# Performance work log

Measured on AMD Instinct MI355X. Metric: run time of the kernel, lower is better.

## Reference

```python
import jax, jax.numpy as jnp
import numpy as np
from jax import lax

IN_DIM = 128
B, H, W = 4, 64, 64


def setup_inputs() -> dict:
    key = jax.random.key(0)
    ks = jax.random.split(key, 11)
    C = IN_DIM
    c8 = C // 8
    s = lambda k, shape, scale: jax.random.normal(k, shape, dtype=jnp.float32) * scale
    return {
        "x": s(ks[0], (B, C, H, W), 1.0),
        "x_forward": s(ks[1], (B, C, H, W), 1.0),
        "x_backward": s(ks[2], (B, C, H, W), 1.0),
        # 1x1 conv weights stored as [out, in]
        "Wq": s(ks[3], (c8, C), C ** -0.5),
        "bq": jnp.zeros((c8,), jnp.float32),
        "Wk": s(ks[4], (c8, C), C ** -0.5),
        "bk": jnp.zeros((c8,), jnp.float32),
        "Wv": s(ks[5], (C, C), C ** -0.5),
        "bv": jnp.zeros((C,), jnp.float32),
        # 3x3 conv weight [out=C, in=2C, kh, kw]
        "Wf": s(ks[6], (C, 2 * C, 3, 3), (2 * C * 9) ** -0.5),
        "bf": jnp.zeros((C,), jnp.float32),
    }


def _conv1x1(x, w, b):
    # x: [B,C,H,W], w: [O,C] -> [B,O,H,W]
    return jnp.einsum("bchw,oc->bohw", x, w) + b[None, :, None, None]


def reference(x, x_forward, x_backward, Wq, bq, Wk, bk, Wv, bv, Wf, bf):
    Bb, C, Hh, Ww = x.shape
    HW = Hh * Ww
    query = _conv1x1(x_forward, Wq, bq).reshape(Bb, -1, HW)   # [B,c8,HW]
    key = _conv1x1(x, Wk, bk).reshape(Bb, -1, HW)             # [B,c8,HW]
    value = _conv1x1(x_backward, Wv, bv).reshape(Bb, C, HW)   # [B,C,HW]

    # att_score[b, k_pos, q_pos] = key[b,:,k_pos] . query[b,:,q_pos]
    att_score = jnp.einsum("bck,bcq->bkq", key, query)        # [B,HW,HW]
    max_value = jnp.max(att_score, axis=-1)                   # [B,HW]
    idx = jnp.argmax(att_score, axis=-1)                      # [B,HW] int

    selected_value = jnp.take_along_axis(value, idx[:, None, :], axis=2)
    selected_value = selected_value.reshape(Bb, C, Hh, Ww)
    max_value = max_value.reshape(Bb, 1, Hh, Ww)

    front_res = jnp.concatenate([x, selected_value], axis=1)  # [B,2C,H,W]
    front_res = lax.conv_general_dilated(
        front_res, Wf, window_strides=(1, 1), padding="SAME",
        dimension_numbers=("NCHW", "OIHW", "NCHW"),
    ) + bf[None, :, None, None]
    front_res = front_res * max_value
    return x + front_res
```

## Files before the change

kernel.cpp:

```cpp
#include <hip/hip_runtime.h>

#define HW 4096
#define CC 128
#define MARGIN 2e-3f

typedef unsigned short ushort_t;
typedef unsigned int uint_t;
typedef __attribute__((ext_vector_type(8))) short short8;
typedef __attribute__((ext_vector_type(4))) float f32x4;

__device__ __forceinline__ float dot4(float4 a, float4 b) {
    return (a.x*b.x + a.y*b.y) + (a.z*b.z + a.w*b.w);
}

__device__ __forceinline__ ushort_t f2bf(float f) {
    union { float f; uint_t u; } cv; cv.f = f;
    uint_t r = cv.u + 0x7fffu + ((cv.u >> 16) & 1u);
    return (ushort_t)(r >> 16);
}

__device__ __forceinline__ float bf2f(ushort_t h) {
    union { uint_t u; float f; } cv; cv.u = ((uint_t)h) << 16;
    return cv.f;
}

__device__ __forceinline__ void store16(ushort_t* dst, const ushort_t* s) {
    union { ushort_t s[8]; uint4 v; } a, b;
    #pragma unroll
    for (int j = 0; j < 8; j++) { a.s[j] = s[j]; b.s[j] = s[8+j]; }
    *(uint4*)dst = a.v;
    *(uint4*)(dst + 8) = b.v;
}

__device__ __forceinline__ void gl2lds16(const ushort_t* g, ushort_t* l) {
    __builtin_amdgcn_global_load_lds(
        (const __attribute__((address_space(1))) unsigned int*)g,
        (__attribute__((address_space(3))) unsigned int*)l, 16, 0, 0);
}

__global__ __launch_bounds__(256) void prep_kernel(
    const float* __restrict__ x, const float* __restrict__ xf, const float* __restrict__ xb,
    const float* __restrict__ Wq, const float* __restrict__ bq,
    const float* __restrict__ Wk, const float* __restrict__ bk,
    const float* __restrict__ Wv, const float* __restrict__ bv,
    const float* __restrict__ Wf,
    float* __restrict__ Qt, float* __restrict__ Kt, float* __restrict__ V,
    ushort_t* __restrict__ Qs, ushort_t* __restrict__ KB,
    ushort_t* __restrict__ xsel, ushort_t* __restrict__ Wt)
{
    __shared__ __align__(16) unsigned char smem[16704];
    int bid = blockIdx.x;
    int tid = threadIdx.x;

    if (bid < 32) {
        float* sW = (float*)smem;
        float* sB = sW + 2048;
        bool isQ = bid < 16;
        const float* src  = isQ ? xf : x;
        const float* W    = isQ ? Wq : Wk;
        const float* bias = isQ ? bq : bk;
        int sub = bid & 15;
        int b = sub >> 2, pt = sub & 3;
        for (int e = tid; e < 2048; e += 256) sW[e] = W[e];
        if (tid < 16) sB[tid] = bias[tid];
        __syncthreads();

        int p = pt*1024 + tid*4;
        const float* sp = src + (size_t)b * CC * HW + p;

        float4 acc[16];
        #pragma unroll
        for (int o = 0; o < 16; o++) { float bb = sB[o]; acc[o] = make_float4(bb,bb,bb,bb); }

        for (int c4 = 0; c4 < 128; c4 += 4) {
            float4 x0 = *(const float4*)&sp[(c4+0)*HW];
            float4 x1 = *(const float4*)&sp[(c4+1)*HW];
            float4 x2 = *(const float4*)&sp[(c4+2)*HW];
            float4 x3 = *(const float4*)&sp[(c4+3)*HW];
            #pragma unroll
            for (int o = 0; o < 16; o++) {
                float4 w = *(const float4*)&sW[o*128 + c4];
                acc[o].x += w.x*x0.x + w.y*x1.x + w.z*x2.x + w.w*x3.x;
                acc[o].y += w.x*x0.y + w.y*x1.y + w.z*x2.y + w.w*x3.y;
                acc[o].z += w.x*x0.z + w.y*x1.z + w.z*x2.z + w.w*x3.z;
                acc[o].w += w.x*x0.w + w.y*x1.w + w.z*x2.w + w.w*x3.w;
            }
        }

        float* dstF = isQ ? Qt : Kt;
        int pg = b*4096 + p;
        #pragma unroll
        for (int pp = 0; pp < 4; pp++) {
            float vd[16];
            #pragma unroll
            for (int o = 0; o < 16; o++)
                vd[o] = (pp==0) ? acc[o].x : (pp==1) ? acc[o].y : (pp==2) ? acc[o].z : acc[o].w;
            float4* df = (float4*)(dstF + (size_t)(pg + pp)*16);
            df[0] = make_float4(vd[0],vd[1],vd[2],vd[3]);
            df[1] = make_float4(vd[4],vd[5],vd[6],vd[7]);
            df[2] = make_float4(vd[8],vd[9],vd[10],vd[11]);
            df[3] = make_float4(vd[12],vd[13],vd[14],vd[15]);
            ushort_t h[16], m[16], l[16];
            #pragma unroll
            for (int d = 0; d < 16; d++) {
                h[d] = f2bf(vd[d]);
                float r1 = vd[d] - bf2f(h[d]);
                m[d] = f2bf(r1);
                l[d] = f2bf(r1 - bf2f(m[d]));
            }
            if (isQ) {
                ushort_t* o_ = Qs + (size_t)(pg + pp)*64;
                store16(o_,      h);
                store16(o_ + 16, m);
                store16(o_ + 32, h);
                store16(o_ + 48, l);
            } else {
                int k = p + pp;
                int u = b*256 + (k >> 4);
                int n = k & 15;
                ushort_t* o_ = KB + (size_t)u*1536 + n*32;
                store16(o_,        h); store16(o_ + 16,   h);
                store16(o_ + 512,  m); store16(o_ + 528,  m);
                store16(o_ + 1024, l); store16(o_ + 1040, h);
            }
        }
    } else if (bid < 160) {
        float* sW = (float*)smem;
        int vbid = bid - 32;
        int b = vbid >> 5, og = (vbid >> 3) & 3, pt = vbid & 7;
        for (int e = tid; e < 4096; e += 256) sW[e] = Wv[og*4096 + e];
        __syncthreads();

        int oz = tid >> 7, pz = tid & 127;
        int p = pt*512 + pz*4;
        const float* sp = xb + (size_t)b * CC * HW + p;

        float4 acc[16];
        #pragma unroll
        for (int j = 0; j < 16; j++) acc[j] = make_float4(0.f,0.f,0.f,0.f);

        for (int c4 = 0; c4 < 128; c4 += 4) {
            float4 x0 = *(const float4*)&sp[(c4+0)*HW];
            float4 x1 = *(const float4*)&sp[(c4+1)*HW];
            float4 x2 = *(const float4*)&sp[(c4+2)*HW];
            float4 x3 = *(const float4*)&sp[(c4+3)*HW];
            #pragma unroll
            for (int j = 0; j < 16; j++) {
                float4 w = *(const float4*)&sW[(oz*16 + j)*128 + c4];
                acc[j].x += w.x*x0.x + w.y*x1.x + w.z*x2.x + w.w*x3.x;
                acc[j].y += w.x*x0.y + w.y*x1.y + w.z*x2.y + w.w*x3.y;
                acc[j].z += w.x*x0.z + w.y*x1.z + w.z*x2.z + w.w*x3.z;
                acc[j].w += w.x*x0.w + w.y*x1.w + w.z*x2.w + w.w*x3.w;
            }
        }
        #pragma unroll
        for (int j = 0; j < 16; j++) {
            int o = og*32 + oz*16 + j;
            float bb = bv[o];
            float4 r = make_float4(acc[j].x+bb, acc[j].y+bb, acc[j].z+bb, acc[j].w+bb);
            *(float4*)&V[(((size_t)b*CC + o)<<12) + p] = r;
        }
    } else if (bid < 416) {
        ushort_t* sT = (ushort_t*)smem;
        int xbid = bid - 160;
        int b = xbid >> 6, y = xbid & 63;
        int cq = tid >> 6, xx = tid & 63;
        const float* src = x + ((size_t)b << 19) + (y << 6) + xx;
        #pragma unroll 4
        for (int k = 0; k < 32; k++) {
            int c = cq*32 + k;
            sT[xx*130 + c] = f2bf(src[(size_t)c << 12]);
        }
        __syncthreads();
        uint_t* dst = (uint_t*)(xsel + ((size_t)(b*4356 + (y+1)*66 + 1))*256);
        #pragma unroll
        for (int k = 0; k < 16; k++) {
            int idx = k*256 + tid;
            int s = idx >> 6, u = idx & 63;
            uint_t v = *(const uint_t*)&sT[s*130 + u*2];
            dst[s*128 + u] = v;
        }
    } else if (bid < 546) {
        int g = (bid - 416) * 256 + tid;
        if (g < 33280) {
            int b = g / 8320;
            int rem = g - b * 8320;
            int si = rem >> 5;
            int ch = rem & 31;
            int y, xx;
            if (si < 66)      { y = 0;  xx = si; }
            else if (si < 132){ y = 65; xx = si - 66; }
            else { int t = si - 132; y = 1 + (t >> 1); xx = (t & 1) ? 65 : 0; }
            int site = y * 66 + xx;
            uint4* dst = (uint4*)(xsel + ((size_t)(b*4356 + site))*256);
            dst[ch] = make_uint4(0,0,0,0);
        }
    } else {
        int t = (bid - 546) * 256 + tid;
        if (t < 36864) {
            int cg = t & 3;
            int o = (t >> 2) & 31;
            int tc = t >> 7;
            int tap = tc % 9;
            int rest = tc / 9;
            int cb = rest & 7, og = rest >> 3;
            union { ushort_t s[8]; uint4 v; } pk;
            #pragma unroll
            for (int j = 0; j < 8; j++) {
                int ci = cg*8 + j;
                pk.s[j] = f2bf(Wf[(size_t)(og*32 + o)*2304 + (cb*32 + ci)*9 + tap]);
            }
            *(uint4*)(Wt + (size_t)t*8) = pk.v;
        }
    }
}

__global__ __launch_bounds__(512) void att_kernel(
    const ushort_t* __restrict__ Qs, const ushort_t* __restrict__ KB,
    float* __restrict__ pm1, int* __restrict__ pi1, float* __restrict__ pm2)
{
    __shared__ float sM1[64*33];
    __shared__ int   sI1[64*33];
    __shared__ float sM2[64*33];

    int bid = blockIdx.x;
    int qh = bid & 1, kg = (bid >> 1) & 63, b = bid >> 7;
    int tid = threadIdx.x;
    int wave = tid >> 6, lane = tid & 63;
    int l15 = lane & 15, quad = lane >> 4;

    short8 Bf[4][3];
    const ushort_t* kb = KB + ((size_t)((b*256 + kg*4)*3))*512 + l15*32 + quad*8;
    #pragma unroll
    for (int t = 0; t < 4; t++)
        #pragma unroll
        for (int p = 0; p < 3; p++)
            Bf[t][p] = *(const short8*)(kb + (size_t)(t*3 + p)*512);

    const ushort_t* qbase = Qs + ((size_t)(b*4096 + qh*2048 + wave*256 + l15))*64 + quad*8;

    float m1[4], m2[4]; int i1[4];
    #pragma unroll
    for (int t = 0; t < 4; t++) { m1[t] = -1e30f; m2[t] = -1e30f; i1[t] = 0; }

    for (int it = 0; it < 16; it++) {
        const ushort_t* aptr = qbase + it*1024;
        short8 A1 = *(const short8*)aptr;
        short8 A2 = *(const short8*)(aptr + 32);
        f32x4 acc[4];
        #pragma unroll
        for (int t = 0; t < 4; t++) {
            acc[t] = (f32x4)0.f;
            acc[t] = __builtin_amdgcn_mfma_f32_16x16x32_bf16(A1, Bf[t][0], acc[t], 0, 0, 0);
            acc[t] = __builtin_amdgcn_mfma_f32_16x16x32_bf16(A1, Bf[t][1], acc[t], 0, 0, 0);
            acc[t] = __builtin_amdgcn_mfma_f32_16x16x32_bf16(A2, Bf[t][2], acc[t], 0, 0, 0);
        }
        int q0 = qh*2048 + wave*256 + it*16 + quad*4;
        #pragma unroll
        for (int r = 0; r < 4; r++) {
            int cand = q0 + r;
            #pragma unroll
            for (int t = 0; t < 4; t++) {
                float d = acc[t][r];
                float old1 = m1[t];
                bool gt = d > old1;
                m1[t] = gt ? d : old1;
                i1[t] = gt ? cand : i1[t];
                m2[t] = fmaxf(m2[t], fminf(d, old1));
            }
        }
    }

    #pragma unroll
    for (int t = 0; t < 4; t++) {
        int kl_ = t*16 + l15;
        int slot = wave*4 + quad;
        sM1[kl_*33 + slot] = m1[t];
        sI1[kl_*33 + slot] = i1[t];
        sM2[kl_*33 + slot] = m2[t];
    }
    __syncthreads();
    if (tid < 64) {
        float M1 = -1e30f; int I1 = 0x7fffffff;
        for (int s = 0; s < 32; s++) {
            float m = sM1[tid*33 + s]; int i = sI1[tid*33 + s];
            if (m > M1 || (m == M1 && i < I1)) { M1 = m; I1 = i; }
        }
        float M2 = -1e30f;
        for (int s = 0; s < 32; s++) {
            float m = sM1[tid*33 + s]; int i = sI1[tid*33 + s];
            float cnd = (i == I1) ? sM2[tid*33 + s] : m;
            M2 = fmaxf(M2, cnd);
        }
        int out = ((qh*4 + b) << 12) + kg*64 + tid;
        pm1[out] = M1; pi1[out] = I1; pm2[out] = M2;
    }
}

__global__ __launch_bounds__(256) void fixup1_kernel(
    const float* __restrict__ pm1, const int* __restrict__ pi1,
    const float* __restrict__ pm2,
    float* __restrict__ maxv, int* __restrict__ idxv,
    int* __restrict__ gN, int* __restrict__ gList)
{
    int row = blockIdx.x*256 + threadIdx.x;
    int b = row >> 12, k = row & 4095;
    float m1a = pm1[(b<<12)+k];     int i1a = pi1[(b<<12)+k];     float m2a = pm2[(b<<12)+k];
    float m1b = pm1[((4+b)<<12)+k]; int i1b = pi1[((4+b)<<12)+k]; float m2b = pm2[((4+b)<<12)+k];
    float M1, ru; int I1;
    if (m1b > m1a) { M1 = m1b; I1 = i1b; ru = fmaxf(m1a, fmaxf(m2a, m2b)); }
    else           { M1 = m1a; I1 = i1a; ru = fmaxf(m1b, fmaxf(m2a, m2b)); }
    maxv[row] = M1; idxv[row] = I1;
    if (M1 - ru < MARGIN) {
        int p = atomicAdd(gN, 1);
        gList[p] = row;
    }
}

__global__ __launch_bounds__(256) void fixup2_kernel(
    const float* __restrict__ Qt, const float* __restrict__ Kt,
    const int* __restrict__ gN, const int* __restrict__ gList,
    float* __restrict__ maxv, int* __restrict__ idxv)
{
    __shared__ float sRm[256];
    __shared__ int   sRi[256];
    int n = *gN;
    int tid = threadIdx.x;
    for (int e = blockIdx.x; e < n; e += 64) {
        int r2 = gList[e];
        int b2 = r2 >> 12, k2 = r2 & 4095;
        const float4* Kp = (const float4*)(Kt + ((size_t)(b2*4096 + k2))*16);
        float4 ka = Kp[0], kbv = Kp[1], kc = Kp[2], kd = Kp[3];
        const float4* Qp = (const float4*)(Qt + ((size_t)b2*4096)*16);
        float m = -1e30f; int i = 0;
        #pragma unroll 4
        for (int j = 0; j < 16; j++) {
            int q = tid*16 + j;
            float4 qa = Qp[q*4+0], qb = Qp[q*4+1], qc = Qp[q*4+2], qd = Qp[q*4+3];
            float d = (dot4(ka,qa) + dot4(kbv,qb)) + (dot4(kc,qc) + dot4(kd,qd));
            if (d > m) { m = d; i = q; }
        }
        sRm[tid] = m; sRi[tid] = i;
        __syncthreads();
        #pragma unroll
        for (int s = 128; s > 0; s >>= 1) {
            if (tid < s) {
                float mo = sRm[tid+s]; int io = sRi[tid+s];
                if (mo > sRm[tid] || (mo == sRm[tid] && io < sRi[tid])) {
                    sRm[tid] = mo; sRi[tid] = io;
                }
            }
            __syncthreads();
        }
        if (tid == 0) { maxv[r2] = sRm[0]; idxv[r2] = sRi[0]; }
        __syncthreads();
    }
}

__global__ __launch_bounds__(256) void gather_kernel(
    const float* __restrict__ V, const int* __restrict__ idxv,
    ushort_t* __restrict__ xsel)
{
    int bid = blockIdx.x;
    int b = bid >> 6, pt = bid & 63;
    int tid = threadIdx.x;
    int pp = tid >> 2, cq = tid & 3;
    int p = pt*64 + pp;
    int ip = idxv[(b << 12) + p];
    const float* vb = V + ((size_t)b << 19) + ip;
    int site = ((p >> 6) + 1)*66 + (p & 63) + 1;
    ushort_t* dst = xsel + ((size_t)(b*4356 + site))*256 + 128 + cq*32;
    #pragma unroll
    for (int k = 0; k < 4; k++) {
        union { ushort_t s[8]; uint4 v; } pk;
        #pragma unroll
        for (int j = 0; j < 8; j++) {
            int c = cq*32 + k*8 + j;
            pk.s[j] = f2bf(vb[(size_t)c << 12]);
        }
        *(uint4*)(dst + k*8) = pk.v;
    }
}

__global__ __launch_bounds__(256) void conv_kernel(
    const float* __restrict__ x, const ushort_t* __restrict__ xsel,
    const ushort_t* __restrict__ Wt, const float* __restrict__ bf,
    const float* __restrict__ maxv, float* __restrict__ out)
{
    __shared__ __align__(16) ushort_t sIn[336*32];
    __shared__ __align__(16) ushort_t sW[9*32*32];

    int bid = blockIdx.x;
    int og = bid & 3, tx = (bid >> 2) & 3, ty = (bid >> 4) & 3, b = bid >> 6;
    int tid = threadIdx.x;
    int wave = tid >> 6, lane = tid & 63;
    int l15 = lane & 15, quad = lane >> 4;

    const ushort_t* xsel_base = xsel + ((size_t)(b*4356 + (ty*16)*66 + tx*16))*256;
    const ushort_t* wt_base   = Wt + (size_t)og*8*9216;

    f32x4 acc[4][2];
    #pragma unroll
    for (int mi = 0; mi < 4; mi++)
        #pragma unroll
        for (int ni = 0; ni < 2; ni++) acc[mi][ni] = (f32x4)0.f;

    int l4q = lane >> 2, l4 = lane & 3;

    for (int cb = 0; cb < 8; cb++) {
        if (cb) __syncthreads();
        for (int r = wave; r < 21; r += 4) {
            int site = r*16 + l4q;
            int iy = site / 18, ix = site - iy*18;
            const ushort_t* g = xsel_base + (size_t)(iy*66 + ix)*256 + cb*32 + l4*8;
            gl2lds16(g, &sIn[r*512]);
        }
        for (int r = wave; r < 18; r += 4) {
            const ushort_t* g = wt_base + (size_t)cb*9216 + r*512 + lane*8;
            gl2lds16(g, &sW[r*512]);
        }
        __syncthreads();

        #pragma unroll
        for (int tap = 0; tap < 9; tap++) {
            const int dy = tap / 3, dx = tap % 3;
            short8 B0 = *(const short8*)&sW[(tap*32 +      l15)*32 + quad*8];
            short8 B1 = *(const short8*)&sW[(tap*32 + 16 + l15)*32 + quad*8];
            #pragma unroll
            for (int mi = 0; mi < 4; mi++) {
                int row = wave*4 + mi + dy;
                short8 A = *(const short8*)&sIn[(row*18 + l15 + dx)*32 + quad*8];
                acc[mi][0] = __builtin_amdgcn_mfma_f32_16x16x32_bf16(A, B0, acc[mi][0], 0, 0, 0);
                acc[mi][1] = __builtin_amdgcn_mfma_f32_16x16x32_bf16(A, B1, acc[mi][1], 0, 0, 0);
            }
        }
    }

    int y0 = ty*16, x0 = tx*16;
    const float* xb_ = x   + ((size_t)b << 19);
    float*       ob  = out + ((size_t)b << 19);
    const float* mxb = maxv + (b << 12);
    #pragma unroll
    for (int mi = 0; mi < 4; mi++) {
        int y = y0 + wave*4 + mi;
        int p = (y << 6) + x0 + quad*4;
        float4 mv = *(const float4*)&mxb[p];
        #pragma unroll
        for (int ni = 0; ni < 2; ni++) {
            int o = og*32 + ni*16 + l15;
            float bfo = bf[o];
            float4 xv = *(const float4*)&xb_[((size_t)o << 12) + p];
            float4 r;
            r.x = xv.x + mv.x * (acc[mi][ni][0] + bfo);
            r.y = xv.y + mv.y * (acc[mi][ni][1] + bfo);
            r.z = xv.z + mv.z * (acc[mi][ni][2] + bfo);
            r.w = xv.w + mv.w * (acc[mi][ni][3] + bfo);
            *(float4*)&ob[((size_t)o << 12) + p] = r;
        }
    }
}

extern "C" void kernel_launch(void* const* d_in, const int* in_sizes, int n_in,
                              void* d_out, int out_size, void* d_ws, size_t ws_size,
                              hipStream_t stream) {
    (void)in_sizes; (void)n_in; (void)out_size; (void)ws_size;
    const float* x  = (const float*)d_in[0];
    const float* xf = (const float*)d_in[1];
    const float* xb = (const float*)d_in[2];
    const float* Wq = (const float*)d_in[3];
    const float* bq = (const float*)d_in[4];
    const float* Wk = (const float*)d_in[5];
    const float* bk = (const float*)d_in[6];
    const float* Wv = (const float*)d_in[7];
    const float* bv = (const float*)d_in[8];
    const float* Wf = (const float*)d_in[9];
    const float* bf = (const float*)d_in[10];
    float* out = (float*)d_out;

    float* ws   = (float*)d_ws;
    float* Qt   = ws;
    float* Kt   = Qt + 262144;
    float* V    = Kt + 262144;
    float* mx   = V  + 2097152;
    int*   idxv = (int*)(mx + 16384);
    float* pm1  = (float*)(idxv + 16384);
    int*   pi1  = (int*)(pm1 + 32768);
    float* pm2  = (float*)(pi1 + 32768);
    int*   gN   = (int*)(pm2 + 32768);
    int*   gList= gN + 4;
    ushort_t* Qs   = (ushort_t*)(gList + 16384);
    ushort_t* KB   = Qs + 1048576;
    ushort_t* xsel = KB + 1572864;
    ushort_t* Wt   = xsel + 4460544;

    hipMemsetAsync(gN, 0, sizeof(int), stream);
    hipLaunchKernelGGL(prep_kernel,   dim3(690), dim3(256), 0, stream,
                       x, xf, xb, Wq, bq, Wk, bk, Wv, bv, Wf, Qt, Kt, V, Qs, KB, xsel, Wt);
    hipLaunchKernelGGL(att_kernel,    dim3(512), dim3(512), 0, stream, Qs, KB, pm1, pi1, pm2);
    hipLaunchKernelGGL(fixup1_kernel, dim3(64),  dim3(256), 0, stream, pm1, pi1, pm2, mx, idxv, gN, gList);
    hipLaunchKernelGGL(fixup2_kernel, dim3(64),  dim3(256), 0, stream, Qt, Kt, gN, gList, mx, idxv);
    hipLaunchKernelGGL(gather_kernel, dim3(256), dim3(256), 0, stream, V, idxv, xsel);
    hipLaunchKernelGGL(conv_kernel,   dim3(256), dim3(256), 0, stream, x, xsel, Wt, bf, mx, out);
}
```

Before: 207.3 us.

## Move value projection into attention kernel and widen Q/K projection grid

The value 1x1 conv leaves prep_kernel and now runs as 128 extra blocks at the front of the attention kernel, so it overlaps with the attention blocks instead of lengthening the prep stage. The Q/K projection goes from 32 blocks with 4 pixels per thread to 128 blocks with 1 pixel per thread. Its weights are now read straight from global memory rather than staged in LDS. This trades register-level reuse and wider loads for more parallelism in the small prep stage. The V blocks now use 512 threads with float2 loads, which may lower per-thread efficiency.

```diff
diff --git a/kernel.cpp b/kernel.cpp
--- a/kernel.cpp
+++ b/kernel.cpp
@@ -39,12 +39,11 @@
 }
 
 __global__ __launch_bounds__(256) void prep_kernel(
-    const float* __restrict__ x, const float* __restrict__ xf, const float* __restrict__ xb,
+    const float* __restrict__ x, const float* __restrict__ xf,
     const float* __restrict__ Wq, const float* __restrict__ bq,
     const float* __restrict__ Wk, const float* __restrict__ bk,
-    const float* __restrict__ Wv, const float* __restrict__ bv,
     const float* __restrict__ Wf,
-    float* __restrict__ Qt, float* __restrict__ Kt, float* __restrict__ V,
+    float* __restrict__ Qt, float* __restrict__ Kt,
     ushort_t* __restrict__ Qs, ushort_t* __restrict__ KB,
     ushort_t* __restrict__ xsel, ushort_t* __restrict__ Wt)
 {
@@ -52,117 +51,64 @@
     int bid = blockIdx.x;
     int tid = threadIdx.x;
 
-    if (bid < 32) {
-        float* sW = (float*)smem;
-        float* sB = sW + 2048;
-        bool isQ = bid < 16;
+    if (bid < 128) {
+        bool isQ = bid < 64;
         const float* src  = isQ ? xf : x;
         const float* W    = isQ ? Wq : Wk;
         const float* bias = isQ ? bq : bk;
-        int sub = bid & 15;
-        int b = sub >> 2, pt = sub & 3;
-        for (int e = tid; e < 2048; e += 256) sW[e] = W[e];
-        if (tid < 16) sB[tid] = bias[tid];
-        __syncthreads();
-
-        int p = pt*1024 + tid*4;
-        const float* sp = src + (size_t)b * CC * HW + p;
-
-        float4 acc[16];
-        #pragma unroll
-        for (int o = 0; o < 16; o++) { float bb = sB[o]; acc[o] = make_float4(bb,bb,bb,bb); }
+
+        int pg = (bid & 63) * 256 + tid;
+        int b = pg >> 12, p = pg & 4095;
+        const float* sp = src + ((size_t)b << 19) + p;
+
+        float acc[16];
+        #pragma unroll
+        for (int o = 0; o < 16; o++) acc[o] = bias[o];
 
         for (int c4 = 0; c4 < 128; c4 += 4) {
-            float4 x0 = *(const float4*)&sp[(c4+0)*HW];
-            float4 x1 = *(const float4*)&sp[(c4+1)*HW];
-            float4 x2 = *(const float4*)&sp[(c4+2)*HW];
-            float4 x3 = *(const float4*)&sp[(c4+3)*HW];
+            float x0 = sp[(size_t)(c4+0) << 12];
+            float x1 = sp[(size_t)(c4+1) << 12];
+            float x2 = sp[(size_t)(c4+2) << 12];
+            float x3 = sp[(size_t)(c4+3) << 12];
             #pragma unroll
             for (int o = 0; o < 16; o++) {
-                float4 w = *(const float4*)&sW[o*128 + c4];
-                acc[o].x += w.x*x0.x + w.y*x1.x + w.z*x2.x + w.w*x3.x;
-                acc[o].y += w.x*x0.y + w.y*x1.y + w.z*x2.y + w.w*x3.y;
-                acc[o].z += w.x*x0.z + w.y*x1.z + w.z*x2.z + w.w*x3.z;
-                acc[o].w += w.x*x0.w + w.y*x1.w + w.z*x2.w + w.w*x3.w;
+                float4 w = *(const float4*)&W[o*128 + c4];
+                acc[o] += w.x*x0 + w.y*x1 + w.z*x2 + w.w*x3;
             }
         }
 
         float* dstF = isQ ? Qt : Kt;
-        int pg = b*4096 + p;
-        #pragma unroll
-        for (int pp = 0; pp < 4; pp++) {
-            float vd[16];
-            #pragma unroll
-            for (int o = 0; o < 16; o++)
-                vd[o] = (pp==0) ? acc[o].x : (pp==1) ? acc[o].y : (pp==2) ? acc[o].z : acc[o].w;
-            float4* df = (float4*)(dstF + (size_t)(pg + pp)*16);
-            df[0] = make_float4(vd[0],vd[1],vd[2],vd[3]);
-            df[1] = make_float4(vd[4],vd[5],vd[6],vd[7]);
-            df[2] = make_float4(vd[8],vd[9],vd[10],vd[11]);
-            df[3] = make_float4(vd[12],vd[13],vd[14],vd[15]);
-            ushort_t h[16], m[16], l[16];
-            #pragma unroll
-            for (int d = 0; d < 16; d++) {
-                h[d] = f2bf(vd[d]);
-                float r1 = vd[d] - bf2f(h[d]);
-                m[d] = f2bf(r1);
-                l[d] = f2bf(r1 - bf2f(m[d]));
-            }
-            if (isQ) {
-                ushort_t* o_ = Qs + (size_t)(pg + pp)*64;
-                store16(o_,      h);
-                store16(o_ + 16, m);
-                store16(o_ + 32, h);
-                store16(o_ + 48, l);
-            } else {
-                int k = p + pp;
-                int u = b*256 + (k >> 4);
-                int n = k & 15;
-                ushort_t* o_ = KB + (size_t)u*1536 + n*32;
-                store16(o_,        h); store16(o_ + 16,   h);
-                store16(o_ + 512,  m); store16(o_ + 528,  m);
-                store16(o_ + 1024, l); store16(o_ + 1040, h);
-            }
-        }
-    } else if (bid < 160) {
-        float* sW = (float*)smem;
-        int vbid = bid - 32;
-        int b = vbid >> 5, og = (vbid >> 3) & 3, pt = vbid & 7;
-        for (int e = tid; e < 4096; e += 256) sW[e] = Wv[og*4096 + e];
-        __syncthreads();
-
-        int oz = tid >> 7, pz = tid & 127;
-        int p = pt*512 + pz*4;
-        const float* sp = xb + (size_t)b * CC * HW + p;
-
-        float4 acc[16];
-        #pragma unroll
-        for (int j = 0; j < 16; j++) acc[j] = make_float4(0.f,0.f,0.f,0.f);
-
-        for (int c4 = 0; c4 < 128; c4 += 4) {
-            float4 x0 = *(const float4*)&sp[(c4+0)*HW];
-            float4 x1 = *(const float4*)&sp[(c4+1)*HW];
-            float4 x2 = *(const float4*)&sp[(c4+2)*HW];
-            float4 x3 = *(const float4*)&sp[(c4+3)*HW];
-            #pragma unroll
-            for (int j = 0; j < 16; j++) {
-                float4 w = *(const float4*)&sW[(oz*16 + j)*128 + c4];
-                acc[j].x += w.x*x0.x + w.y*x1.x + w.z*x2.x + w.w*x3.x;
-                acc[j].y += w.x*x0.y + w.y*x1.y + w.z*x2.y + w.w*x3.y;
-                acc[j].z += w.x*x0.z + w.y*x1.z + w.z*x2.z + w.w*x3.z;
-                acc[j].w += w.x*x0.w + w.y*x1.w + w.z*x2.w + w.w*x3.w;
-            }
-        }
-        #pragma unroll
-        for (int j = 0; j < 16; j++) {
-            int o = og*32 + oz*16 + j;
-            float bb = bv[o];
-            float4 r = make_float4(acc[j].x+bb, acc[j].y+bb, acc[j].z+bb, acc[j].w+bb);
-            *(float4*)&V[(((size_t)b*CC + o)<<12) + p] = r;
-        }
-    } else if (bid < 416) {
+        float4* df = (float4*)(dstF + (size_t)pg * 16);
+        df[0] = make_float4(acc[0],acc[1],acc[2],acc[3]);
+        df[1] = make_float4(acc[4],acc[5],acc[6],acc[7]);
+        df[2] = make_float4(acc[8],acc[9],acc[10],acc[11]);
+        df[3] = make_float4(acc[12],acc[13],acc[14],acc[15]);
+
+        ushort_t h[16], m[16], l[16];
+        #pragma unroll
+        for (int d = 0; d < 16; d++) {
+            h[d] = f2bf(acc[d]);
+            float r1 = acc[d] - bf2f(h[d]);
+            m[d] = f2bf(r1);
+            l[d] = f2bf(r1 - bf2f(m[d]));
+        }
+        if (isQ) {
+            ushort_t* o_ = Qs + (size_t)pg*64;
+            store16(o_,      h);
+            store16(o_ + 16, m);
+            store16(o_ + 32, h);
+            store16(o_ + 48, l);
+        } else {
+            int u = b*256 + (p >> 4);
+            int n = p & 15;
+            ushort_t* o_ = KB + (size_t)u*1536 + n*32;
+            store16(o_,        h); store16(o_ + 16,   h);
+            store16(o_ + 512,  m); store16(o_ + 528,  m);
+            store16(o_ + 1024, l); store16(o_ + 1040, h);
+        }
+    } else if (bid < 384) {
         ushort_t* sT = (ushort_t*)smem;
-        int xbid = bid - 160;
+        int xbid = bid - 128;
         int b = xbid >> 6, y = xbid & 63;
         int cq = tid >> 6, xx = tid & 63;
         const float* src = x + ((size_t)b << 19) + (y << 6) + xx;
@@ -180,8 +126,8 @@
             uint_t v = *(const uint_t*)&sT[s*130 + u*2];
             dst[s*128 + u] = v;
         }
-    } else if (bid < 546) {
-        int g = (bid - 416) * 256 + tid;
+    } else if (bid < 514) {
+        int g = (bid - 384) * 256 + tid;
         if (g < 33280) {
             int b = g / 8320;
             int rem = g - b * 8320;
@@ -196,7 +142,7 @@
             dst[ch] = make_uint4(0,0,0,0);
         }
     } else {
-        int t = (bid - 546) * 256 + tid;
+        int t = (bid - 514) * 256 + tid;
         if (t < 36864) {
             int cg = t & 3;
             int o = (t >> 2) & 31;
@@ -215,7 +161,9 @@
     }
 }
 
-__global__ __launch_bounds__(512) void att_kernel(
+__global__ __launch_bounds__(512) void attv_kernel(
+    const float* __restrict__ xb, const float* __restrict__ Wv,
+    const float* __restrict__ bv, float* __restrict__ V,
     const ushort_t* __restrict__ Qs, const ushort_t* __restrict__ KB,
     float* __restrict__ pm1, int* __restrict__ pi1, float* __restrict__ pm2)
 {
@@ -224,8 +172,42 @@
     __shared__ float sM2[64*33];
 
     int bid = blockIdx.x;
-    int qh = bid & 1, kg = (bid >> 1) & 63, b = bid >> 7;
     int tid = threadIdx.x;
+
+    if (bid < 128) {
+        int b = bid >> 5, og = (bid >> 3) & 3, pt = bid & 7;
+        int oz = tid >> 8, pz = tid & 255;
+        int p = pt*512 + pz*2;
+        const float* sp = xb + ((size_t)b << 19) + p;
+
+        float2 acc[16];
+        #pragma unroll
+        for (int j = 0; j < 16; j++) acc[j] = make_float2(0.f, 0.f);
+
+        for (int c4 = 0; c4 < 128; c4 += 4) {
+            float2 x0 = *(const float2*)&sp[(size_t)(c4+0) << 12];
+            float2 x1 = *(const float2*)&sp[(size_t)(c4+1) << 12];
+            float2 x2 = *(const float2*)&sp[(size_t)(c4+2) << 12];
+            float2 x3 = *(const float2*)&sp[(size_t)(c4+3) << 12];
+            #pragma unroll
+            for (int j = 0; j < 16; j++) {
+                float4 w = *(const float4*)&Wv[(og*32 + oz*16 + j)*128 + c4];
+                acc[j].x += w.x*x0.x + w.y*x1.x + w.z*x2.x + w.w*x3.x;
+                acc[j].y += w.x*x0.y + w.y*x1.y + w.z*x2.y + w.w*x3.y;
+            }
+        }
+        #pragma unroll
+        for (int j = 0; j < 16; j++) {
+            int o = og*32 + oz*16 + j;
+            float bb = bv[o];
+            float2 r = make_float2(acc[j].x + bb, acc[j].y + bb);
+            *(float2*)&V[(((size_t)b*CC + o)<<12) + p] = r;
+        }
+        return;
+    }
+
+    int abid = bid - 128;
+    int qh = abid & 1, kg = (abid >> 1) & 63, b = abid >> 7;
     int wave = tid >> 6, lane = tid & 63;
     int l15 = lane & 15, quad = lane >> 4;
 
@@ -494,9 +476,10 @@
     ushort_t* Wt   = xsel + 4460544;
 
     hipMemsetAsync(gN, 0, sizeof(int), stream);
-    hipLaunchKernelGGL(prep_kernel,   dim3(690), dim3(256), 0, stream,
-                       x, xf, xb, Wq, bq, Wk, bk, Wv, bv, Wf, Qt, Kt, V, Qs, KB, xsel, Wt);
-    hipLaunchKernelGGL(att_kernel,    dim3(512), dim3(512), 0, stream, Qs, KB, pm1, pi1, pm2);
+    hipLaunchKernelGGL(prep_kernel,   dim3(658), dim3(256), 0, stream,
+                       x, xf, Wq, bq, Wk, bk, Wf, Qt, Kt, Qs, KB, xsel, Wt);
+    hipLaunchKernelGGL(attv_kernel,   dim3(640), dim3(512), 0, stream,
+                       xb, Wv, bv, V, Qs, KB, pm1, pi1, pm2);
     hipLaunchKernelGGL(fixup1_kernel, dim3(64),  dim3(256), 0, stream, pm1, pi1, pm2, mx, idxv, gN, gList);
     hipLaunchKernelGGL(fixup2_kernel, dim3(64),  dim3(256), 0, stream, Qt, Kt, gN, gList, mx, idxv);
     hipLaunchKernelGGL(gather_kernel, dim3(256), dim3(256), 0, stream, V, idxv, xsel);
```

Measured after the change: 215.0 us. 1.04x slower.
